# Kernel optimization log

Measured on AMD Instinct MI355X. Metric: run time of the kernel, lower is better.

The kernel has to match this reference:

```python
import jax, jax.numpy as jnp
import numpy as np

VOCAB = 50000
D = 200
N_CONCEPTS = 100000
B = 256
L = 8


def setup_inputs() -> dict:
    key = jax.random.key(0)
    k1, k2, k3 = jax.random.split(key, 3)
    mention_word_ids = jax.random.randint(k1, (B, L), 0, VOCAB)
    word_embedding = jax.random.normal(k2, (VOCAB, D), dtype=jnp.float32)
    dict_embedding = jax.random.normal(k3, (N_CONCEPTS, D), dtype=jnp.float32)
    return {
        "mention_word_ids": mention_word_ids,
        "word_embedding": word_embedding,
        "dict_embedding": dict_embedding,
    }


def reference(mention_word_ids, word_embedding, dict_embedding):
    # Embedding lookup [B, L, D] then mean-pool over tokens (avg_pool2d over L) -> [B, D]
    mention_rep = jnp.mean(word_embedding[mention_word_ids], axis=1)
    # Cosine similarity: dot / (||m|| * ||c||), denominator clamped at 1e-8
    m_norm = jnp.linalg.norm(mention_rep, axis=1, keepdims=True)        # [B, 1]
    c_norm = jnp.linalg.norm(dict_embedding, axis=1, keepdims=True)     # [N, 1]
    denom = jnp.maximum(m_norm * c_norm.T, 1e-8)                        # [B, N]
    sims = jnp.matmul(mention_rep, dict_embedding.T) / denom            # [B, N]
    values = jnp.max(sims, axis=1)
    indices = jnp.argmax(sims, axis=1)
    return values, indices
```

## Files before the change

kernel.cpp:

```cpp
#include <hip/hip_runtime.h>
#include <math.h>

#define BB 256
#define LL 8
#define DD 200
#define NN 100000
#define BN 32
#define NTILE (NN / BN)
#define NGRAN 28
#define UPT (NGRAN * BN)
#define GRID_SIM 512
#define NCAND 6

typedef __attribute__((ext_vector_type(8))) __bf16 bf16x8;
typedef __attribute__((ext_vector_type(16))) float f32x16;

__device__ __forceinline__ unsigned f2bf(float x) {
  unsigned u = __float_as_uint(x);
  u = (u + 0x7fffu + ((u >> 16) & 1u)) >> 16;
  return u;
}
__device__ __forceinline__ unsigned pk(float a, float b) {
  return f2bf(a) | (f2bf(b) << 16);
}
__device__ __forceinline__ bool better(float a, int ia, float b, int ib) {
  return (a > b) || (a == b && ia < ib);
}

__device__ __forceinline__ void glds16(const void* g, void* l) {
  __builtin_amdgcn_global_load_lds(
      (const __attribute__((address_space(1))) unsigned int*)g,
      (__attribute__((address_space(3))) unsigned int*)l, 16, 0, 0);
}

__global__ __launch_bounds__(256) void convert_kernel(
    const float* __restrict__ dict, uint4* __restrict__ dictbf) {
  __shared__ uint4 T[UPT];
  int tile = blockIdx.x;
  int tid = threadIdx.x;
  int row = tid >> 3, part = tid & 7;
  const float* src = dict + (size_t)(tile * BN + row) * DD;

  float4 f[8];
  int gl[4] = {part, part + 8, part + 16, 24};
  int ng = (part == 0) ? 4 : 3;
  float sq = 0.f;
#pragma unroll
  for (int i = 0; i < 4; ++i) {
    if (i < ng) {
      int g = gl[i];
      float4 a = *(const float4*)(src + g * 8);
      float4 b = *(const float4*)(src + g * 8 + 4);
      f[2 * i] = a; f[2 * i + 1] = b;
      sq += a.x * a.x + a.y * a.y + a.z * a.z + a.w * a.w;
      sq += b.x * b.x + b.y * b.y + b.z * b.z + b.w * b.w;
    }
  }
  sq += __shfl_xor(sq, 1); sq += __shfl_xor(sq, 2); sq += __shfl_xor(sq, 4);
  float rs = 1.0f / fmaxf(sqrtf(sq), 1e-8f);
#pragma unroll
  for (int i = 0; i < 4; ++i) {
    if (i < ng) {
      int g = gl[i];
      float4 a = f[2 * i], b = f[2 * i + 1];
      uint4 u;
      u.x = pk(a.x * rs, a.y * rs); u.y = pk(a.z * rs, a.w * rs);
      u.z = pk(b.x * rs, b.y * rs); u.w = pk(b.z * rs, b.w * rs);
      T[g * BN + row] = u;
    }
  }
  if (part >= 1 && part <= 3)
    T[(24 + part) * BN + row] = make_uint4(0, 0, 0, 0);
  __syncthreads();
  size_t base = (size_t)tile * UPT;
#pragma unroll
  for (int e = 0; e < 4; ++e) {
    int idx = tid + e * 256;
    if (idx < UPT) dictbf[base + idx] = T[idx];
  }
}

__global__ __launch_bounds__(256) void prep_kernel(
    const int* __restrict__ ids, const float* __restrict__ we,
    float* __restrict__ repf, unsigned short* __restrict__ abf,
    float* __restrict__ mnorm) {
  int m = blockIdx.x, d = threadIdx.x;
  __shared__ float red[4];
  float r = 0.f;
  if (d < DD) {
    int base = m * LL;
#pragma unroll
    for (int l2 = 0; l2 < LL; ++l2) r += we[(size_t)ids[base + l2] * DD + d];
    r *= 0.125f;
    repf[m * DD + d] = r;
  }
  if (d < NGRAN * 8) {
    int g = d >> 3, wo = d & 7;
    abf[(g * 256 + m) * 8 + wo] = (unsigned short)f2bf(d < DD ? r : 0.f);
  }
  float sq = (d < DD) ? r * r : 0.f;
#pragma unroll
  for (int off = 32; off; off >>= 1) sq += __shfl_down(sq, off);
  if ((threadIdx.x & 63) == 0) red[threadIdx.x >> 6] = sq;
  __syncthreads();
  if (threadIdx.x == 0) mnorm[m] = sqrtf(red[0] + red[1] + red[2] + red[3]);
}

__global__ __launch_bounds__(512, 4) void sim_kernel(
    const uint4* __restrict__ dictbf, const uint4* __restrict__ abfT,
    float4* __restrict__ partial) {
  __shared__ uint4 Bs[2][UPT];

  int tid = threadIdx.x;
  int w = tid >> 6, l = tid & 63;
  int ln = l & 31, kh = l >> 5;
  int m = w * 32 + ln;

  uint4 areg[14];
#pragma unroll
  for (int j = 0; j < 14; ++j) areg[j] = abfT[(2 * j + kh) * 256 + m];

  float v1 = -INFINITY, v2 = -INFINITY;
  int i1 = 0x7fffffff, i2 = 0x7fffffff;

  int t0 = blockIdx.x;
  if (w < 7) {
#pragma unroll
    for (int i = 0; i < 2; ++i) {
      int u = w * 128 + i * 64;
      glds16(dictbf + (size_t)t0 * UPT + u + l, (char*)&Bs[0][0] + u * 16);
    }
  }

  int cur = 0;
  for (int t = t0; t < NTILE; t += GRID_SIM) {
    int tn = t + GRID_SIM;
    bool hn = tn < NTILE;
    if (hn && w < 7) {
#pragma unroll
      for (int i = 0; i < 2; ++i) {
        int u = w * 128 + i * 64;
        glds16(dictbf + (size_t)tn * UPT + u + l,
               (char*)&Bs[cur ^ 1][0] + u * 16);
      }
    }
    if (hn) asm volatile("s_waitcnt vmcnt(2)" ::: "memory");
    else    asm volatile("s_waitcnt vmcnt(0)" ::: "memory");
    __builtin_amdgcn_s_barrier();
    __builtin_amdgcn_sched_barrier(0);

    f32x16 acc;
#pragma unroll
    for (int i = 0; i < 16; ++i) acc[i] = 0.f;
    const uint4* B = Bs[cur];
#pragma unroll
    for (int j = 0; j < 14; ++j) {
      bf16x8 a = __builtin_bit_cast(bf16x8, B[(2 * j + kh) * 32 + ln]);
      acc = __builtin_amdgcn_mfma_f32_32x32x16_bf16(
          a, __builtin_bit_cast(bf16x8, areg[j]), acc, 0, 0, 0);
    }

    int n0 = t * BN + 4 * kh;
#pragma unroll
    for (int r = 0; r < 16; ++r) {
      int n = n0 + (r & 3) + 8 * (r >> 2);
      float v = acc[r];
      if (v > v1) { v2 = v1; i2 = i1; v1 = v; i1 = n; }
      else if (v > v2) { v2 = v; i2 = n; }
    }
    __builtin_amdgcn_s_barrier();
    cur ^= 1;
  }

  float w1 = __shfl_xor(v1, 32); int j1 = __shfl_xor(i1, 32);
  float w2 = __shfl_xor(v2, 32); int j2 = __shfl_xor(i2, 32);
  float o1, o2; int oi1, oi2;
  if (better(w1, j1, v1, i1)) {
    bool tt = better(v1, i1, w2, j2);
    o1 = w1; oi1 = j1; o2 = tt ? v1 : w2; oi2 = tt ? i1 : j2;
  } else {
    bool tt = better(w1, j1, v2, i2);
    o1 = v1; oi1 = i1; o2 = tt ? w1 : v2; oi2 = tt ? j1 : i2;
  }
  if (kh == 0)
    partial[(size_t)m * GRID_SIM + blockIdx.x] =
        make_float4(o1, __int_as_float(oi1), o2, __int_as_float(oi2));
}

__global__ __launch_bounds__(256) void final_kernel(
    const float* __restrict__ dict, const float* __restrict__ repf,
    const float* __restrict__ mnorm, const float4* __restrict__ partial,
    float* __restrict__ out) {
  int m = blockIdx.x, tid = threadIdx.x;
  __shared__ float repL[DD];
  __shared__ int seln[NCAND];
  __shared__ float wv[4]; __shared__ int wi[4];
  __shared__ float finv[NCAND]; __shared__ int finn[NCAND];
  if (tid < DD) repL[tid] = repf[m * DD + tid];
  __syncthreads();

  const float4* pm = partial + (size_t)m * GRID_SIM;
  float cv1[2], cv2[2]; int ci1[2], ci2[2];
#pragma unroll
  for (int e = 0; e < 2; ++e) {
    float4 E = pm[tid + e * 256];
    cv1[e] = E.x; ci1[e] = __float_as_int(E.y);
    cv2[e] = E.z; ci2[e] = __float_as_int(E.w);
  }

  for (int r = 0; r < NCAND; ++r) {
    float bv = -INFINITY; int bi = 0x7fffffff;
#pragma unroll
    for (int e = 0; e < 2; ++e) {
      bool ex1 = false, ex2 = false;
      for (int j = 0; j < r; ++j) {
        int s = seln[j];
        ex1 |= (s == ci1[e]); ex2 |= (s == ci2[e]);
      }
      if (!ex1 && better(cv1[e], ci1[e], bv, bi)) { bv = cv1[e]; bi = ci1[e]; }
      if (!ex2 && better(cv2[e], ci2[e], bv, bi)) { bv = cv2[e]; bi = ci2[e]; }
    }
#pragma unroll
    for (int off = 1; off < 64; off <<= 1) {
      float ov = __shfl_xor(bv, off); int oi = __shfl_xor(bi, off);
      if (better(ov, oi, bv, bi)) { bv = ov; bi = oi; }
    }
    if ((tid & 63) == 0) { wv[tid >> 6] = bv; wi[tid >> 6] = bi; }
    __syncthreads();
    if (tid == 0) {
      float Bv = wv[0]; int Bi = wi[0];
#pragma unroll
      for (int q = 1; q < 4; ++q)
        if (better(wv[q], wi[q], Bv, Bi)) { Bv = wv[q]; Bi = wi[q]; }
      seln[r] = Bi;
    }
    __syncthreads();
  }

  int g = tid >> 5, lane = tid & 31;
  int n = (g < NCAND) ? seln[g] : -1;
  float s1 = 0.f, s2 = 0.f;
  if (n >= 0) {
    for (int d = lane; d < DD; d += 32) {
      float b = dict[(size_t)n * DD + d];
      s1 += repL[d] * b; s2 += b * b;
    }
  }
#pragma unroll
  for (int off = 1; off < 32; off <<= 1) {
    s1 += __shfl_xor(s1, off); s2 += __shfl_xor(s2, off);
  }
  if (lane == 0 && g < NCAND) {
    finv[g] = (n >= 0) ? s1 / fmaxf(mnorm[m] * sqrtf(s2), 1e-8f) : -INFINITY;
    finn[g] = n;
  }
  __syncthreads();
  if (tid == 0) {
    float Bv = finv[0]; int Bi = finn[0];
#pragma unroll
    for (int q = 1; q < NCAND; ++q)
      if (better(finv[q], finn[q], Bv, Bi)) { Bv = finv[q]; Bi = finn[q]; }
    out[m] = Bv;
    out[BB + m] = (float)Bi;
  }
}

extern "C" void kernel_launch(void* const* d_in, const int* in_sizes, int n_in,
                              void* d_out, int out_size, void* d_ws, size_t ws_size,
                              hipStream_t stream) {
  const int* ids = (const int*)d_in[0];
  const float* we = (const float*)d_in[1];
  const float* dict = (const float*)d_in[2];
  float* out = (float*)d_out;

  char* ws = (char*)d_ws;
  uint4* dictbf = (uint4*)ws;
  unsigned short* abf = (unsigned short*)(ws + 44800000);
  float* repf  = (float*)(ws + 44914688);
  float* mnorm = (float*)(ws + 45119488);
  float4* partial = (float4*)(ws + 45120512);

  convert_kernel<<<NTILE, 256, 0, stream>>>(dict, dictbf);
  prep_kernel<<<BB, 256, 0, stream>>>(ids, we, repf, abf, mnorm);
  sim_kernel<<<GRID_SIM, 512, 0, stream>>>(dictbf, (const uint4*)abf, partial);
  final_kernel<<<BB, 256, 0, stream>>>(dict, repf, mnorm, partial, out);
}
```

Measured before the change: 56.68 us.

## Fuse dictionary normalize-and-convert into similarity kernel with register-staged prefetch

Removes the separate convert kernel that wrote a normalized bf16 copy of the dictionary to workspace. The sim kernel now loads fp32 dictionary rows directly, computes row norms, scales, packs to bf16 and writes them into an XOR-swizzled LDS double buffer. The next tile's loads are issued before the MFMA work, which cuts one full read and write pass over the dictionary plus a launch. In exchange the sim kernel takes on extra ALU, shuffle and register pressure, and its loads go through registers instead of direct-to-LDS.

Result: faster. 45.67 us (-19.4%).

```diff
diff --git a/kernel.cpp b/kernel.cpp
--- a/kernel.cpp
+++ b/kernel.cpp
@@ -8,7 +8,6 @@
 #define BN 32
 #define NTILE (NN / BN)
 #define NGRAN 28
-#define UPT (NGRAN * BN)
 #define GRID_SIM 512
 #define NCAND 6
 
@@ -26,58 +25,8 @@
 __device__ __forceinline__ bool better(float a, int ia, float b, int ib) {
   return (a > b) || (a == b && ia < ib);
 }
-
-__device__ __forceinline__ void glds16(const void* g, void* l) {
-  __builtin_amdgcn_global_load_lds(
-      (const __attribute__((address_space(1))) unsigned int*)g,
-      (__attribute__((address_space(3))) unsigned int*)l, 16, 0, 0);
-}
-
-__global__ __launch_bounds__(256) void convert_kernel(
-    const float* __restrict__ dict, uint4* __restrict__ dictbf) {
-  __shared__ uint4 T[UPT];
-  int tile = blockIdx.x;
-  int tid = threadIdx.x;
-  int row = tid >> 3, part = tid & 7;
-  const float* src = dict + (size_t)(tile * BN + row) * DD;
-
-  float4 f[8];
-  int gl[4] = {part, part + 8, part + 16, 24};
-  int ng = (part == 0) ? 4 : 3;
-  float sq = 0.f;
-#pragma unroll
-  for (int i = 0; i < 4; ++i) {
-    if (i < ng) {
-      int g = gl[i];
-      float4 a = *(const float4*)(src + g * 8);
-      float4 b = *(const float4*)(src + g * 8 + 4);
-      f[2 * i] = a; f[2 * i + 1] = b;
-      sq += a.x * a.x + a.y * a.y + a.z * a.z + a.w * a.w;
-      sq += b.x * b.x + b.y * b.y + b.z * b.z + b.w * b.w;
-    }
-  }
-  sq += __shfl_xor(sq, 1); sq += __shfl_xor(sq, 2); sq += __shfl_xor(sq, 4);
-  float rs = 1.0f / fmaxf(sqrtf(sq), 1e-8f);
-#pragma unroll
-  for (int i = 0; i < 4; ++i) {
-    if (i < ng) {
-      int g = gl[i];
-      float4 a = f[2 * i], b = f[2 * i + 1];
-      uint4 u;
-      u.x = pk(a.x * rs, a.y * rs); u.y = pk(a.z * rs, a.w * rs);
-      u.z = pk(b.x * rs, b.y * rs); u.w = pk(b.z * rs, b.w * rs);
-      T[g * BN + row] = u;
-    }
-  }
-  if (part >= 1 && part <= 3)
-    T[(24 + part) * BN + row] = make_uint4(0, 0, 0, 0);
-  __syncthreads();
-  size_t base = (size_t)tile * UPT;
-#pragma unroll
-  for (int e = 0; e < 4; ++e) {
-    int idx = tid + e * 256;
-    if (idx < UPT) dictbf[base + idx] = T[idx];
-  }
+__device__ __forceinline__ float dot4(float4 f) {
+  return f.x * f.x + f.y * f.y + f.z * f.z + f.w * f.w;
 }
 
 __global__ __launch_bounds__(256) void prep_kernel(
@@ -107,9 +56,9 @@
 }
 
 __global__ __launch_bounds__(512, 4) void sim_kernel(
-    const uint4* __restrict__ dictbf, const uint4* __restrict__ abfT,
+    const float* __restrict__ dict, const uint4* __restrict__ abfT,
     float4* __restrict__ partial) {
-  __shared__ uint4 Bs[2][UPT];
+  __shared__ uint4 Bs[2][NGRAN * BN];
 
   int tid = threadIdx.x;
   int w = tid >> 6, l = tid & 63;
@@ -120,33 +69,58 @@
 #pragma unroll
   for (int j = 0; j < 14; ++j) areg[j] = abfT[(2 * j + kh) * 256 + m];
 
+  int row = tid >> 4, part = tid & 15;
+  const bool extra = (part < 2);
+  int g0i = part >> 1, h = part & 1;
+
+  if (tid < 192) {
+    int buf = tid / 96, u = tid % 96;
+    int g = 25 + u / 32, r = u & 31;
+    Bs[buf][g * 32 + (r ^ (g & 7))] = make_uint4(0, 0, 0, 0);
+  }
+
   float v1 = -INFINITY, v2 = -INFINITY;
   int i1 = 0x7fffffff, i2 = 0x7fffffff;
 
   int t0 = blockIdx.x;
-  if (w < 7) {
-#pragma unroll
-    for (int i = 0; i < 2; ++i) {
-      int u = w * 128 + i * 64;
-      glds16(dictbf + (size_t)t0 * UPT + u + l, (char*)&Bs[0][0] + u * 16);
-    }
-  }
+  {
+    const float* src = dict + (size_t)(t0 * BN + row) * DD;
+    float4 f0 = *(const float4*)(src + 4 * part);
+    float4 f1 = *(const float4*)(src + 64 + 4 * part);
+    float4 f2 = *(const float4*)(src + 128 + 4 * part);
+    float4 f3 = extra ? *(const float4*)(src + 192 + 4 * part)
+                      : make_float4(0.f, 0.f, 0.f, 0.f);
+    float sq = dot4(f0) + dot4(f1) + dot4(f2) + dot4(f3);
+    sq += __shfl_xor(sq, 1); sq += __shfl_xor(sq, 2);
+    sq += __shfl_xor(sq, 4); sq += __shfl_xor(sq, 8);
+    float rs = 1.0f / fmaxf(sqrtf(sq), 1e-8f);
+    uint2* B2 = (uint2*)&Bs[0][0];
+    B2[(g0i * 32 + (row ^ (g0i & 7))) * 2 + h] =
+        make_uint2(pk(f0.x * rs, f0.y * rs), pk(f0.z * rs, f0.w * rs));
+    int ga = 8 + g0i;
+    B2[(ga * 32 + (row ^ (ga & 7))) * 2 + h] =
+        make_uint2(pk(f1.x * rs, f1.y * rs), pk(f1.z * rs, f1.w * rs));
+    int gb = 16 + g0i;
+    B2[(gb * 32 + (row ^ (gb & 7))) * 2 + h] =
+        make_uint2(pk(f2.x * rs, f2.y * rs), pk(f2.z * rs, f2.w * rs));
+    if (extra)
+      B2[(24 * 32 + (row ^ 0)) * 2 + part] =
+          make_uint2(pk(f3.x * rs, f3.y * rs), pk(f3.z * rs, f3.w * rs));
+  }
+  __syncthreads();
 
   int cur = 0;
   for (int t = t0; t < NTILE; t += GRID_SIM) {
-    int tn = t + GRID_SIM;
-    bool hn = tn < NTILE;
-    if (hn && w < 7) {
-#pragma unroll
-      for (int i = 0; i < 2; ++i) {
-        int u = w * 128 + i * 64;
-        glds16(dictbf + (size_t)tn * UPT + u + l,
-               (char*)&Bs[cur ^ 1][0] + u * 16);
-      }
-    }
-    if (hn) asm volatile("s_waitcnt vmcnt(2)" ::: "memory");
-    else    asm volatile("s_waitcnt vmcnt(0)" ::: "memory");
-    __builtin_amdgcn_s_barrier();
+    bool hn = (t + GRID_SIM) < NTILE;
+    float4 f0, f1, f2, f3;
+    if (hn) {
+      const float* src = dict + (size_t)((t + GRID_SIM) * BN + row) * DD;
+      f0 = *(const float4*)(src + 4 * part);
+      f1 = *(const float4*)(src + 64 + 4 * part);
+      f2 = *(const float4*)(src + 128 + 4 * part);
+      f3 = extra ? *(const float4*)(src + 192 + 4 * part)
+                 : make_float4(0.f, 0.f, 0.f, 0.f);
+    }
     __builtin_amdgcn_sched_barrier(0);
 
     f32x16 acc;
@@ -155,7 +129,8 @@
     const uint4* B = Bs[cur];
 #pragma unroll
     for (int j = 0; j < 14; ++j) {
-      bf16x8 a = __builtin_bit_cast(bf16x8, B[(2 * j + kh) * 32 + ln]);
+      int g = 2 * j + kh;
+      bf16x8 a = __builtin_bit_cast(bf16x8, B[g * 32 + (ln ^ (g & 7))]);
       acc = __builtin_amdgcn_mfma_f32_32x32x16_bf16(
           a, __builtin_bit_cast(bf16x8, areg[j]), acc, 0, 0, 0);
     }
@@ -168,7 +143,26 @@
       if (v > v1) { v2 = v1; i2 = i1; v1 = v; i1 = n; }
       else if (v > v2) { v2 = v; i2 = n; }
     }
-    __builtin_amdgcn_s_barrier();
+
+    if (hn) {
+      float sq = dot4(f0) + dot4(f1) + dot4(f2) + dot4(f3);
+      sq += __shfl_xor(sq, 1); sq += __shfl_xor(sq, 2);
+      sq += __shfl_xor(sq, 4); sq += __shfl_xor(sq, 8);
+      float rs = 1.0f / fmaxf(sqrtf(sq), 1e-8f);
+      uint2* B2 = (uint2*)&Bs[cur ^ 1][0];
+      B2[(g0i * 32 + (row ^ (g0i & 7))) * 2 + h] =
+          make_uint2(pk(f0.x * rs, f0.y * rs), pk(f0.z * rs, f0.w * rs));
+      int ga = 8 + g0i;
+      B2[(ga * 32 + (row ^ (ga & 7))) * 2 + h] =
+          make_uint2(pk(f1.x * rs, f1.y * rs), pk(f1.z * rs, f1.w * rs));
+      int gb = 16 + g0i;
+      B2[(gb * 32 + (row ^ (gb & 7))) * 2 + h] =
+          make_uint2(pk(f2.x * rs, f2.y * rs), pk(f2.z * rs, f2.w * rs));
+      if (extra)
+        B2[(24 * 32 + row) * 2 + part] =
+            make_uint2(pk(f3.x * rs, f3.y * rs), pk(f3.z * rs, f3.w * rs));
+    }
+    __syncthreads();
     cur ^= 1;
   }
 
@@ -274,14 +268,12 @@
   float* out = (float*)d_out;
 
   char* ws = (char*)d_ws;
-  uint4* dictbf = (uint4*)ws;
-  unsigned short* abf = (unsigned short*)(ws + 44800000);
-  float* repf  = (float*)(ws + 44914688);
-  float* mnorm = (float*)(ws + 45119488);
-  float4* partial = (float4*)(ws + 45120512);
-
-  convert_kernel<<<NTILE, 256, 0, stream>>>(dict, dictbf);
+  unsigned short* abf = (unsigned short*)ws;
+  float* repf  = (float*)(ws + 114688);
+  float* mnorm = (float*)(ws + 319488);
+  float4* partial = (float4*)(ws + 320512);
+
   prep_kernel<<<BB, 256, 0, stream>>>(ids, we, repf, abf, mnorm);
-  sim_kernel<<<GRID_SIM, 512, 0, stream>>>(dictbf, (const uint4*)abf, partial);
+  sim_kernel<<<GRID_SIM, 512, 0, stream>>>(dict, (const uint4*)abf, partial);
   final_kernel<<<BB, 256, 0, stream>>>(dict, repf, mnorm, partial, out);
 }
```
